# Kernel optimization log

Measured on AMD Instinct MI355X. Metric: run time of the kernel, lower is better.

The kernel has to match this reference:

```python
import jax, jax.numpy as jnp
import numpy as np
import itertools

FS, C_SOUND, NMICS, NTDOAS, MAX_TAU, TRACKS = 24000, 343, 4, 6, 6, 5
B, T, TR, NCLS = 64, 500, 5, 13
NLOGIT = 2 * MAX_TAU + 1  # 13 TDOA classes
IGNORE = -100
_PAIRS = np.array([(m1, m2) for m1 in range(NMICS) for m2 in range(m1 + 1, NMICS)])  # [6,2]
_PERMS = np.array(list(itertools.permutations(range(TRACKS))))  # [120,5]


def _mic_locs():
    coords = [[0.042, 45, 35], [0.042, -45, -35], [0.042, 135, -35], [0.042, -135, 35]]
    locs = []
    for rad, azi, ele in coords:
        azi, ele = np.deg2rad(azi), np.deg2rad(ele)
        locs.append([rad * np.cos(azi) * np.cos(ele), rad * np.sin(azi) * np.cos(ele), rad * np.sin(ele)])
    return np.array(locs, dtype=np.float32)


def setup_inputs() -> dict:
    key = jax.random.key(0)
    k1, k2, k3, k4 = jax.random.split(key, 4)
    pred = jax.random.normal(k1, (B, T, NLOGIT, TR, NTDOAS), dtype=jnp.float32)
    active = (jax.random.uniform(k2, (B, T, TR, NCLS)) < 0.06).astype(jnp.float32)
    doa = jax.random.normal(k3, (B, T, TR, 3, NCLS), dtype=jnp.float32)
    doa = doa / jnp.linalg.norm(doa, axis=3, keepdims=True)
    dist = jax.random.uniform(k4, (B, T, TR, NCLS), minval=1.0, maxval=5.0, dtype=jnp.float32)
    target = jnp.concatenate([active[:, :, :, None, :], doa, dist[:, :, :, None, :]], axis=3)
    return {"pred": pred, "target": target, "mic_locs": jnp.asarray(_mic_locs())}


def _tdoa_targets(target, mic_locs):
    # target: [B,T,Tr,5,C] -> int32 class targets [B,T,Tr,NTDOAS]
    Bs, Ts, Tr, _, C = target.shape
    active = target[:, :, :, 0, :] != 0                                   # [B,T,Tr,C]
    src = jnp.moveaxis(target[:, :, :, 1:4, :] * target[:, :, :, 4:5, :], 3, -1)  # [B,T,Tr,C,3]
    d = jnp.linalg.norm(src[..., None, :] - mic_locs[None, None, None, None], axis=-1)  # [B,T,Tr,C,4]
    tdoa = d[..., _PAIRS[:, 0]] - d[..., _PAIRS[:, 1]]                    # [B,T,Tr,C,6]
    cls = jnp.round(tdoa * FS / C_SOUND).astype(jnp.int32) + MAX_TAU      # in [0, 2*max_tau]
    # pack first Tr active sources (tr-major, class-minor order) into track slots
    act_flat = active.reshape(Bs, Ts, Tr * C)
    cls_flat = cls.reshape(Bs, Ts, Tr * C, NTDOAS)
    order = jnp.argsort(jnp.logical_not(act_flat).astype(jnp.int32), axis=-1, stable=True)
    sel = order[:, :, :Tr]                                                # [B,T,Tr]
    vals = jnp.take_along_axis(cls_flat, sel[..., None], axis=2)          # [B,T,Tr,6]
    slot_ok = jnp.arange(Tr)[None, None, :] < act_flat.sum(-1)[..., None]
    return jnp.where(slot_ok[..., None], vals, IGNORE)


def reference(pred, target, mic_locs):
    tdoas = _tdoa_targets(target, mic_locs)                               # [B,T,Tr,P]
    Bs, Ts, CL, Tr, P = pred.shape
    N = Bs * Ts * P
    tgt = jnp.transpose(tdoas, (0, 1, 3, 2)).reshape(N, Tr)               # [N,Tr]
    logits = jnp.transpose(pred, (0, 1, 4, 2, 3)).reshape(N, CL, Tr)      # [N,CL,Tr]
    logp = jax.nn.log_softmax(logits, axis=1)
    valid = tgt != IGNORE
    safe = jnp.where(valid, tgt, 0)
    idx = jnp.broadcast_to(safe[:, :, None], (N, Tr, Tr))
    ce = jnp.take_along_axis(logp, idx, axis=1)                           # ce[n,i,j] = logp[n, tgt[n,i], j]
    loss_mat = jnp.where(valid[:, :, None], -ce, 0.0)                     # ignore_index -> 0 loss
    cost = loss_mat[:, np.arange(Tr)[None, :], _PERMS].mean(-1)           # [N,120]
    loss = cost.min(axis=1).mean()
    best = jnp.take(jnp.asarray(_PERMS), cost.argmin(axis=1), axis=0)     # [N,Tr]
    pred_cls = logits.argmax(axis=1)                                      # [N,Tr]
    tgt_perm = jnp.take_along_axis(tgt, best, axis=1)
    vp = tgt_perm != IGNORE
    n_pred = vp.sum()
    correct = ((pred_cls == tgt_perm) & vp).sum()
    acc = jnp.where(n_pred > 0, correct / jnp.maximum(n_pred, 1), 0.0).astype(jnp.float32)
    return loss, acc
```

## Files before the change

### kernel.cpp

```cpp
#include <hip/hip_runtime.h>
#include <hip/hip_bf16.h>
#include <math.h>

#define NCELLS 32000
#define NP_ 6
#define IGN (-100)
#define MAIN_BLOCKS 750
#define SCLS_BYTES ((size_t)NCELLS * NP_ * 8)

struct PermTable { int p[120][5]; };
constexpr PermTable make_perms() {
    PermTable t{};
    for (int i = 0; i < 120; ++i) {
        int avail[5] = {0, 1, 2, 3, 4};
        int rem = i;
        const int f[5] = {24, 6, 2, 1, 1};
        for (int k = 0; k < 5; ++k) {
            int d = rem / f[k];
            rem = rem % f[k];
            t.p[i][k] = avail[d];
            for (int m = d; m < 4 - k; ++m) avail[m] = avail[m + 1];
        }
    }
    return t;
}
__device__ constexpr PermTable PT = make_perms();

__global__ __launch_bounds__(320) void tdoa_scan(
        const float* __restrict__ target, const float* __restrict__ mic,
        char* __restrict__ scls) {
    __shared__ int cnt[64][5];
    const int j = threadIdx.x;
    const int cellL = j / 5, tr = j - cellL * 5;
    const int cell = blockIdx.x * 64 + cellL;
    const float* __restrict__ tg = target + (size_t)cell * 325 + tr * 65;

    float fl[13];
#pragma unroll
    for (int c = 0; c < 13; ++c) fl[c] = tg[c];
    int mycnt = 0;
#pragma unroll
    for (int c = 0; c < 13; ++c) mycnt += (fl[c] != 0.0f) ? 1 : 0;
    cnt[cellL][tr] = mycnt;
    __syncthreads();

    int base = 0, total = 0;
#pragma unroll
    for (int t = 0; t < 5; ++t) {
        int v = cnt[cellL][t];
        total += v;
        if (t < tr) base += v;
    }

    char* __restrict__ dst = scls + (size_t)cell * 48;
    if (tr == 0) {
        for (int s = (total < 5 ? total : 5); s < 5; ++s)
#pragma unroll
            for (int p = 0; p < 6; ++p) dst[p * 8 + s] = (char)IGN;
    }

    float mx[4], my[4], mz[4];
#pragma unroll
    for (int m = 0; m < 4; ++m) {
        mx[m] = mic[m * 3 + 0];
        my[m] = mic[m * 3 + 1];
        mz[m] = mic[m * 3 + 2];
    }

    int slot = base;
#pragma unroll
    for (int c = 0; c < 13; ++c) {
        if (fl[c] != 0.0f) {
            if (slot < 5) {
                float dist = tg[52 + c];
                float sx = tg[13 + c] * dist;
                float sy = tg[26 + c] * dist;
                float sz = tg[39 + c] * dist;
                float d[4];
#pragma unroll
                for (int m = 0; m < 4; ++m) {
                    float dx = sx - mx[m], dy = sy - my[m], dz = sz - mz[m];
                    d[m] = sqrtf(dx * dx + dy * dy + dz * dz);
                }
                const int Q0[6] = {0, 0, 0, 1, 1, 2};
                const int Q1[6] = {1, 2, 3, 2, 3, 3};
#pragma unroll
                for (int q = 0; q < 6; ++q) {
                    float td = (d[Q0[q]] - d[Q1[q]]) * (24000.0f / 343.0f);
                    int cls = (int)rintf(td) + 6;
                    cls = cls < 0 ? 0 : (cls > 12 ? 12 : cls);
                    dst[q * 8 + slot] = (char)cls;
                }
            }
            ++slot;
        }
    }
}

__global__ __launch_bounds__(256, 4) void tdoa_main(
        const float* __restrict__ pred, const char* __restrict__ scls,
        float* __restrict__ costp, int* __restrict__ vpp, int* __restrict__ crp) {
    const int tid = blockIdx.x * 256 + threadIdx.x;
    const int cell = tid / 6, p = tid - cell * 6;
    const float* __restrict__ L = pred + (size_t)cell * 390 + p;

    const unsigned long long su =
        *(const unsigned long long*)(scls + (size_t)tid * 8);

    float lse[5];
    int amax[5];
#pragma unroll
    for (int tr = 0; tr < 5; ++tr) {
        float v[13];
#pragma unroll
        for (int c = 0; c < 13; ++c) v[c] = L[c * 30 + tr * 6];
        float m = v[0];
        int am = 0;
#pragma unroll
        for (int c = 1; c < 13; ++c) {
            if (v[c] > m) { m = v[c]; am = c; }
        }
        float s = 0.0f;
#pragma unroll
        for (int c = 0; c < 13; ++c) s += __expf(v[c] - m);
        lse[tr] = m + __logf(s);
        amax[tr] = am;
    }

    float lm[5][5];
#pragma unroll
    for (int slot = 0; slot < 5; ++slot) {
        int tcs = (int)(char)((su >> (slot * 8)) & 0xffULL);
        bool val = (tcs != IGN);
        int tcc = val ? tcs : 0;
        tcc = min(max(tcc, 0), 12);
#pragma unroll
        for (int tr = 0; tr < 5; ++tr) {
            float g = L[tcc * 30 + tr * 6];
            lm[slot][tr] = val ? (lse[tr] - g) : 0.0f;
        }
    }

    float best = 1e30f;
    int bi = 0;
#pragma unroll
    for (int i = 0; i < 120; ++i) {
        float c = lm[0][PT.p[i][0]] + lm[1][PT.p[i][1]] + lm[2][PT.p[i][2]]
                + lm[3][PT.p[i][3]] + lm[4][PT.p[i][4]];
        if (c < best) { best = c; bi = i; }
    }
    float mycost = best * (1.0f / 5.0f);

    int vp = 0, cr = 0;
#pragma unroll
    for (int k = 0; k < 5; ++k) {
        int slot = PT.p[bi][k];
        int tcs = (int)(char)((su >> (slot * 8)) & 0xffULL);
        if (tcs != IGN) {
            ++vp;
            if (amax[k] == tcs) ++cr;
        }
    }

    float rc = mycost;
    int rv = vp, rr = cr;
#pragma unroll
    for (int off = 32; off > 0; off >>= 1) {
        rc += __shfl_down(rc, off, 64);
        rv += __shfl_down(rv, off, 64);
        rr += __shfl_down(rr, off, 64);
    }
    __shared__ float sf[4];
    __shared__ int sv[4], sc2[4];
    const int wave = threadIdx.x >> 6, lane = threadIdx.x & 63;
    if (lane == 0) { sf[wave] = rc; sv[wave] = rv; sc2[wave] = rr; }
    __syncthreads();
    if (threadIdx.x == 0) {
        costp[blockIdx.x] = sf[0] + sf[1] + sf[2] + sf[3];
        vpp[blockIdx.x]   = sv[0] + sv[1] + sv[2] + sv[3];
        crp[blockIdx.x]   = sc2[0] + sc2[1] + sc2[2] + sc2[3];
    }
}

__global__ __launch_bounds__(256) void tdoa_final(
        const float* __restrict__ costp, const int* __restrict__ vpp,
        const int* __restrict__ crp, float* __restrict__ out) {
    __shared__ float sf[4];
    __shared__ int sv[4], sc[4];
    int j = threadIdx.x;
    float c = 0.0f;
    int v = 0, r = 0;
    for (int i = j; i < MAIN_BLOCKS; i += 256) {
        c += costp[i];
        v += vpp[i];
        r += crp[i];
    }
#pragma unroll
    for (int off = 32; off > 0; off >>= 1) {
        c += __shfl_down(c, off, 64);
        v += __shfl_down(v, off, 64);
        r += __shfl_down(r, off, 64);
    }
    int wave = j >> 6, lane = j & 63;
    if (lane == 0) { sf[wave] = c; sv[wave] = v; sc[wave] = r; }
    __syncthreads();
    if (j == 0) {
        float tc = sf[0] + sf[1] + sf[2] + sf[3];
        int tv = sv[0] + sv[1] + sv[2] + sv[3];
        int trr = sc[0] + sc[1] + sc[2] + sc[3];
        out[0] = tc / (float)(NCELLS * NP_);
        out[1] = (tv > 0) ? ((float)trr / (float)tv) : 0.0f;
    }
}

extern "C" void kernel_launch(void* const* d_in, const int* in_sizes, int n_in,
                              void* d_out, int out_size, void* d_ws, size_t ws_size,
                              hipStream_t stream) {
    const float* pred   = (const float*)d_in[0];
    const float* target = (const float*)d_in[1];
    const float* mic    = (const float*)d_in[2];
    float* out = (float*)d_out;

    char*  scls  = (char*)d_ws;
    float* costp = (float*)((char*)d_ws + SCLS_BYTES);
    int*   vpp   = (int*)((char*)d_ws + SCLS_BYTES + MAIN_BLOCKS * 4);
    int*   crp   = (int*)((char*)d_ws + SCLS_BYTES + MAIN_BLOCKS * 8);

    tdoa_scan<<<NCELLS / 64, 320, 0, stream>>>(target, mic, scls);
    tdoa_main<<<MAIN_BLOCKS, 256, 0, stream>>>(pred, scls, costp, vpp, crp);
    tdoa_final<<<1, 256, 0, stream>>>(costp, vpp, crp, out);
}
```

Measured before the change: 143.2 us.

## Fuse TDOA target scan into main loss kernel via shared memory

Merges the target-class scan kernel and the permutation-loss kernel into one kernel with 64 cells per block and 384 threads. The per-cell TDOA classes now go through shared memory instead of a global workspace, which removes a kernel launch and the global write and read of the class array. In exchange, the scan phase leaves 64 threads idle and uses divergent __syncthreads branches, and the launch_bounds occupancy hint of the old main kernel is dropped.

```diff
diff --git a/kernel.cpp b/kernel.cpp
--- a/kernel.cpp
+++ b/kernel.cpp
@@ -5,8 +5,9 @@
 #define NCELLS 32000
 #define NP_ 6
 #define IGN (-100)
-#define MAIN_BLOCKS 750
-#define SCLS_BYTES ((size_t)NCELLS * NP_ * 8)
+#define CPB 64
+#define NBLK (NCELLS / CPB)
+#define THREADS 384
 
 struct PermTable { int p[120][5]; };
 constexpr PermTable make_perms() {
@@ -26,86 +27,87 @@
 }
 __device__ constexpr PermTable PT = make_perms();
 
-__global__ __launch_bounds__(320) void tdoa_scan(
-        const float* __restrict__ target, const float* __restrict__ mic,
-        char* __restrict__ scls) {
-    __shared__ int cnt[64][5];
+__global__ __launch_bounds__(THREADS) void tdoa_fused(
+        const float* __restrict__ pred, const float* __restrict__ target,
+        const float* __restrict__ mic,
+        float* __restrict__ costp, int* __restrict__ vpp, int* __restrict__ crp) {
+    __shared__ int cnt[CPB][5];
+    __shared__ int scls[CPB][NP_][5];
     const int j = threadIdx.x;
-    const int cellL = j / 5, tr = j - cellL * 5;
-    const int cell = blockIdx.x * 64 + cellL;
-    const float* __restrict__ tg = target + (size_t)cell * 325 + tr * 65;
-
-    float fl[13];
-#pragma unroll
-    for (int c = 0; c < 13; ++c) fl[c] = tg[c];
-    int mycnt = 0;
-#pragma unroll
-    for (int c = 0; c < 13; ++c) mycnt += (fl[c] != 0.0f) ? 1 : 0;
-    cnt[cellL][tr] = mycnt;
+    const int blk = blockIdx.x;
+
+    if (j < CPB * 5) {
+        const int cellL = j / 5, tr = j - cellL * 5;
+        const int cell = blk * CPB + cellL;
+        const float* __restrict__ tg = target + (size_t)cell * 325 + tr * 65;
+
+        float fl[13];
+#pragma unroll
+        for (int c = 0; c < 13; ++c) fl[c] = tg[c];
+        int mycnt = 0;
+#pragma unroll
+        for (int c = 0; c < 13; ++c) mycnt += (fl[c] != 0.0f) ? 1 : 0;
+        cnt[cellL][tr] = mycnt;
+        __syncthreads();
+
+        int base = 0, total = 0;
+#pragma unroll
+        for (int t = 0; t < 5; ++t) {
+            int v = cnt[cellL][t];
+            total += v;
+            if (t < tr) base += v;
+        }
+
+        if (tr == 0) {
+            for (int s = (total < 5 ? total : 5); s < 5; ++s)
+#pragma unroll
+                for (int p = 0; p < 6; ++p) scls[cellL][p][s] = IGN;
+        }
+
+        float mx[4], my[4], mz[4];
+#pragma unroll
+        for (int m = 0; m < 4; ++m) {
+            mx[m] = mic[m * 3 + 0];
+            my[m] = mic[m * 3 + 1];
+            mz[m] = mic[m * 3 + 2];
+        }
+
+        int slot = base;
+#pragma unroll
+        for (int c = 0; c < 13; ++c) {
+            if (fl[c] != 0.0f) {
+                if (slot < 5) {
+                    float dist = tg[52 + c];
+                    float sx = tg[13 + c] * dist;
+                    float sy = tg[26 + c] * dist;
+                    float sz = tg[39 + c] * dist;
+                    float d[4];
+#pragma unroll
+                    for (int m = 0; m < 4; ++m) {
+                        float dx = sx - mx[m], dy = sy - my[m], dz = sz - mz[m];
+                        d[m] = sqrtf(dx * dx + dy * dy + dz * dz);
+                    }
+                    const int Q0[6] = {0, 0, 0, 1, 1, 2};
+                    const int Q1[6] = {1, 2, 3, 2, 3, 3};
+#pragma unroll
+                    for (int q = 0; q < 6; ++q) {
+                        float td = (d[Q0[q]] - d[Q1[q]]) * (24000.0f / 343.0f);
+                        int cls = (int)rintf(td) + 6;
+                        cls = cls < 0 ? 0 : (cls > 12 ? 12 : cls);
+                        scls[cellL][q][slot] = cls;
+                    }
+                }
+                ++slot;
+            }
+        }
+    } else {
+        __syncthreads();
+    }
     __syncthreads();
 
-    int base = 0, total = 0;
-#pragma unroll
-    for (int t = 0; t < 5; ++t) {
-        int v = cnt[cellL][t];
-        total += v;
-        if (t < tr) base += v;
-    }
-
-    char* __restrict__ dst = scls + (size_t)cell * 48;
-    if (tr == 0) {
-        for (int s = (total < 5 ? total : 5); s < 5; ++s)
-#pragma unroll
-            for (int p = 0; p < 6; ++p) dst[p * 8 + s] = (char)IGN;
-    }
-
-    float mx[4], my[4], mz[4];
-#pragma unroll
-    for (int m = 0; m < 4; ++m) {
-        mx[m] = mic[m * 3 + 0];
-        my[m] = mic[m * 3 + 1];
-        mz[m] = mic[m * 3 + 2];
-    }
-
-    int slot = base;
-#pragma unroll
-    for (int c = 0; c < 13; ++c) {
-        if (fl[c] != 0.0f) {
-            if (slot < 5) {
-                float dist = tg[52 + c];
-                float sx = tg[13 + c] * dist;
-                float sy = tg[26 + c] * dist;
-                float sz = tg[39 + c] * dist;
-                float d[4];
-#pragma unroll
-                for (int m = 0; m < 4; ++m) {
-                    float dx = sx - mx[m], dy = sy - my[m], dz = sz - mz[m];
-                    d[m] = sqrtf(dx * dx + dy * dy + dz * dz);
-                }
-                const int Q0[6] = {0, 0, 0, 1, 1, 2};
-                const int Q1[6] = {1, 2, 3, 2, 3, 3};
-#pragma unroll
-                for (int q = 0; q < 6; ++q) {
-                    float td = (d[Q0[q]] - d[Q1[q]]) * (24000.0f / 343.0f);
-                    int cls = (int)rintf(td) + 6;
-                    cls = cls < 0 ? 0 : (cls > 12 ? 12 : cls);
-                    dst[q * 8 + slot] = (char)cls;
-                }
-            }
-            ++slot;
-        }
-    }
-}
-
-__global__ __launch_bounds__(256, 4) void tdoa_main(
-        const float* __restrict__ pred, const char* __restrict__ scls,
-        float* __restrict__ costp, int* __restrict__ vpp, int* __restrict__ crp) {
-    const int tid = blockIdx.x * 256 + threadIdx.x;
-    const int cell = tid / 6, p = tid - cell * 6;
-    const float* __restrict__ L = pred + (size_t)cell * 390 + p;
-
-    const unsigned long long su =
-        *(const unsigned long long*)(scls + (size_t)tid * 8);
+    const int cellL = j / NP_, p = j - cellL * NP_;
+    const float* __restrict__ L =
+        pred + (size_t)(blk * CPB + cellL) * 390 + p;
 
     float lse[5];
     int amax[5];
@@ -127,12 +129,15 @@
         amax[tr] = am;
     }
 
+    int tcs[5];
+#pragma unroll
+    for (int slot = 0; slot < 5; ++slot) tcs[slot] = scls[cellL][p][slot];
+
     float lm[5][5];
 #pragma unroll
     for (int slot = 0; slot < 5; ++slot) {
-        int tcs = (int)(char)((su >> (slot * 8)) & 0xffULL);
-        bool val = (tcs != IGN);
-        int tcc = val ? tcs : 0;
+        bool val = (tcs[slot] != IGN);
+        int tcc = val ? tcs[slot] : 0;
         tcc = min(max(tcc, 0), 12);
 #pragma unroll
         for (int tr = 0; tr < 5; ++tr) {
@@ -155,10 +160,10 @@
 #pragma unroll
     for (int k = 0; k < 5; ++k) {
         int slot = PT.p[bi][k];
-        int tcs = (int)(char)((su >> (slot * 8)) & 0xffULL);
-        if (tcs != IGN) {
+        int tc = tcs[slot];
+        if (tc != IGN) {
             ++vp;
-            if (amax[k] == tcs) ++cr;
+            if (amax[k] == tc) ++cr;
         }
     }
 
@@ -170,15 +175,19 @@
         rv += __shfl_down(rv, off, 64);
         rr += __shfl_down(rr, off, 64);
     }
-    __shared__ float sf[4];
-    __shared__ int sv[4], sc2[4];
-    const int wave = threadIdx.x >> 6, lane = threadIdx.x & 63;
+    __shared__ float sf[6];
+    __shared__ int sv[6], sc2[6];
+    const int wave = j >> 6, lane = j & 63;
     if (lane == 0) { sf[wave] = rc; sv[wave] = rv; sc2[wave] = rr; }
     __syncthreads();
-    if (threadIdx.x == 0) {
-        costp[blockIdx.x] = sf[0] + sf[1] + sf[2] + sf[3];
-        vpp[blockIdx.x]   = sv[0] + sv[1] + sv[2] + sv[3];
-        crp[blockIdx.x]   = sc2[0] + sc2[1] + sc2[2] + sc2[3];
+    if (j == 0) {
+        float c = 0.0f;
+        int v = 0, r = 0;
+#pragma unroll
+        for (int w = 0; w < 6; ++w) { c += sf[w]; v += sv[w]; r += sc2[w]; }
+        costp[blk] = c;
+        vpp[blk] = v;
+        crp[blk] = r;
     }
 }
 
@@ -190,7 +199,7 @@
     int j = threadIdx.x;
     float c = 0.0f;
     int v = 0, r = 0;
-    for (int i = j; i < MAIN_BLOCKS; i += 256) {
+    for (int i = j; i < NBLK; i += 256) {
         c += costp[i];
         v += vpp[i];
         r += crp[i];
@@ -221,12 +230,10 @@
     const float* mic    = (const float*)d_in[2];
     float* out = (float*)d_out;
 
-    char*  scls  = (char*)d_ws;
-    float* costp = (float*)((char*)d_ws + SCLS_BYTES);
-    int*   vpp   = (int*)((char*)d_ws + SCLS_BYTES + MAIN_BLOCKS * 4);
-    int*   crp   = (int*)((char*)d_ws + SCLS_BYTES + MAIN_BLOCKS * 8);
-
-    tdoa_scan<<<NCELLS / 64, 320, 0, stream>>>(target, mic, scls);
-    tdoa_main<<<MAIN_BLOCKS, 256, 0, stream>>>(pred, scls, costp, vpp, crp);
+    float* costp = (float*)d_ws;
+    int*   vpp   = (int*)((char*)d_ws + NBLK * 4);
+    int*   crp   = (int*)((char*)d_ws + NBLK * 8);
+
+    tdoa_fused<<<NBLK, THREADS, 0, stream>>>(pred, target, mic, costp, vpp, crp);
     tdoa_final<<<1, 256, 0, stream>>>(costp, vpp, crp, out);
 }
```

After: 135.5 us. 1.06x faster.
